# Performance work log

Measured on AMD Instinct MI355X. Metric: run time of the kernel, lower is better.

The kernel has to match this reference:

```python
import jax, jax.numpy as jnp
import numpy as np

N, E, G = 4096, 16384, 128   # nodes, edges, graphs
IN, H, ED = 64, 64, 16       # in_dim, hidden, edge_dim


def _lin(key, fan_in, fan_out):
    return jax.random.normal(key, (fan_in, fan_out), dtype=jnp.float32) * (fan_in ** -0.5)


def setup_inputs() -> dict:
    key = jax.random.key(0)
    ks = jax.random.split(key, 32)
    inp = {
        "x": jax.random.normal(ks[0], (N, IN), dtype=jnp.float32),
        "edge_index": jax.random.randint(ks[1], (2, E), 0, N, dtype=jnp.int32),
        "edge_attr": jax.random.normal(ks[2], (E, ED), dtype=jnp.float32),
        "batch": jnp.sort(jax.random.randint(ks[3], (N,), 0, G, dtype=jnp.int32)),
    }
    ki = 4
    dims = [(IN, H), (H, H), (H, H)]  # (in_channels, out_channels) per layer
    for l, (ic, oc) in enumerate(dims):
        hd = ic * oc  # edge-MLP width = hidden * in_channels
        inp[f"l{l}_w1"] = _lin(ks[ki], ED, hd); ki += 1
        inp[f"l{l}_b1"] = jnp.zeros((hd,), dtype=jnp.float32)
        inp[f"l{l}_w2"] = _lin(ks[ki], hd, hd); ki += 1
        inp[f"l{l}_b2"] = jnp.zeros((hd,), dtype=jnp.float32)
        inp[f"l{l}_root"] = _lin(ks[ki], ic, oc); ki += 1
        inp[f"l{l}_bias"] = jnp.zeros((oc,), dtype=jnp.float32)
    return inp


def _nnconv(x, src, dst, edge_attr, w1, b1, w2, b2, root, bias, ic, oc):
    # per-edge weight matrix Theta(e): [E, ic, oc]
    h = jax.nn.relu(edge_attr @ w1 + b1)
    theta = (h @ w2 + b2).reshape(-1, ic, oc)
    # gather source features, per-edge bmm, scatter-mean to target
    msg = jnp.einsum("ei,eio->eo", x[src], theta)
    agg = jax.ops.segment_sum(msg, dst, num_segments=N)
    cnt = jax.ops.segment_sum(jnp.ones((msg.shape[0],), msg.dtype), dst, num_segments=N)
    agg = agg / jnp.maximum(cnt, 1.0)[:, None]
    return agg + x @ root + bias


def reference(x, edge_index, edge_attr, batch,
              l0_w1, l0_b1, l0_w2, l0_b2, l0_root, l0_bias,
              l1_w1, l1_b1, l1_w2, l1_b2, l1_root, l1_bias,
              l2_w1, l2_b1, l2_w2, l2_b2, l2_root, l2_bias):
    src, dst = edge_index[0], edge_index[1]
    layers = [
        (l0_w1, l0_b1, l0_w2, l0_b2, l0_root, l0_bias, IN, H),
        (l1_w1, l1_b1, l1_w2, l1_b2, l1_root, l1_bias, H, H),
        (l2_w1, l2_b1, l2_w2, l2_b2, l2_root, l2_bias, H, H),
    ]
    h = x
    for (w1, b1, w2, b2, root, bias, ic, oc) in layers:
        h = jax.nn.relu(_nnconv(h, src, dst, edge_attr, w1, b1, w2, b2, root, bias, ic, oc))
        # dropout is identity in eval mode
    # global mean pool over graphs
    s = jax.ops.segment_sum(h, batch, num_segments=G)
    c = jax.ops.segment_sum(jnp.ones((N,), h.dtype), batch, num_segments=G)
    return s / jnp.maximum(c, 1.0)[:, None]
```

## Files before the change

kernel.cpp:

```cpp
#include <hip/hip_runtime.h>
#include <hip/hip_bf16.h>

#define NN 4096
#define EE 16384
#define GG 128
#define EDIM 16
#define HD 4096

#define NGROUPS 64
#define GK 8
#define KSUBS 64
#define MAXT 40
#define MAXSLOT (MAXT * 16)
#define MAXTW 5
#define SYHALF (64 * 64 * 8)

typedef __attribute__((ext_vector_type(8))) short short8;
typedef __attribute__((ext_vector_type(4))) float float4v;

static __device__ inline unsigned short f2b(float f) {
    unsigned u = __float_as_uint(f);
    unsigned r = u + 0x7fff + ((u >> 16) & 1);
    return (unsigned short)(r >> 16);
}

static __device__ inline unsigned pk2(float a, float b) {
    __hip_bfloat162 p = __float22bfloat162_rn(make_float2(a, b));
    return *(unsigned*)&p;
}

__global__ void hker(const float* __restrict__ ea, const float* __restrict__ w1,
                     const float* __restrict__ b1, unsigned short* __restrict__ hB) {
    __shared__ float sea[16 * 16];
    const int tid = threadIdx.x;
    const int j = blockIdx.x * 256 + tid;
    const int e0 = blockIdx.y * 16;
    float w[16];
#pragma unroll
    for (int k = 0; k < 16; ++k) w[k] = w1[k * HD + j];
    const float b = b1[j];
    sea[tid] = ea[e0 * EDIM + tid];
    __syncthreads();
#pragma unroll 4
    for (int el = 0; el < 16; ++el) {
        float a = b;
#pragma unroll
        for (int k = 0; k < 16; ++k) a += sea[el * 16 + k] * w[k];
        hB[(size_t)(e0 + el) * HD + j] = f2b(fmaxf(a, 0.f));
    }
}

__global__ void wperm(const float* __restrict__ w2, unsigned short* __restrict__ W2q) {
    __shared__ float t[64 * 65];
    const int k = blockIdx.x;
    const int tid = threadIdx.x;
    const int o = tid & 63, r4 = tid >> 6;
#pragma unroll
    for (int it = 0; it < 16; ++it) {
        int i = it * 4 + r4;
        t[i * 65 + o] = w2[(size_t)k * HD + i * 64 + o];
    }
    __syncthreads();
    const int o2 = tid >> 2, q = tid & 3;
    const int ss = k >> 3, kk = k & 7;
    size_t base = ((size_t)(ss * 512 + kk * 64 + o2)) * 64 + q * 16;
    unsigned int buf[8];
#pragma unroll
    for (int j = 0; j < 8; ++j)
        buf[j] = pk2(t[(q * 16 + 2 * j) * 65 + o2], t[(q * 16 + 2 * j + 1) * 65 + o2]);
    *(uint4*)(&W2q[base]) = make_uint4(buf[0], buf[1], buf[2], buf[3]);
    *(uint4*)(&W2q[base + 8]) = make_uint4(buf[4], buf[5], buf[6], buf[7]);
}

__global__ void count_edges(const int* __restrict__ src, const int* __restrict__ dst,
                            int* __restrict__ cnt_src, float* __restrict__ cnt_dst) {
    const int e = blockIdx.x * 256 + threadIdx.x;
    atomicAdd(&cnt_src[src[e]], 1);
    atomicAdd(&cnt_dst[dst[e]], 1.f);
}

__global__ void build_layout(const int* __restrict__ cnt_src, int* __restrict__ node_slot_base,
                             int* __restrict__ tile_cluster, int* __restrict__ group_ntiles) {
    const int g = threadIdx.x;
    int nt = 0;
    int slot = g * MAXSLOT;
    for (int c = 0; c < 16; ++c) {
        int d = 0;
        for (int j = 0; j < 4; ++j) {
            int n = g * 64 + c * 4 + j;
            node_slot_base[n] = slot + d;
            d += cnt_src[n];
        }
        int tcnt = (d + 15) >> 4;
        if (nt + tcnt > MAXT) tcnt = MAXT - nt;
        for (int j = 0; j < tcnt; ++j) tile_cluster[g * MAXT + nt + j] = c;
        nt += tcnt;
        slot += tcnt * 16;
    }
    group_ntiles[g] = nt;
}

__global__ void fill_slots(const int* __restrict__ src, const int* __restrict__ dst,
                           int* __restrict__ fill, const int* __restrict__ node_slot_base,
                           int* __restrict__ slot_info) {
    const int e = blockIdx.x * 256 + threadIdx.x;
    const int n = src[e];
    const int pos = atomicAdd(&fill[n], 1);
    const int s = node_slot_base[n] + pos;
    const int g = n >> 6;
    if (s < g * MAXSLOT + MAXSLOT)
        slot_info[s] = e | ((n & 3) << 14) | (dst[e] << 16);
}

__global__ void xb_ker(const float* __restrict__ xcur, const float* __restrict__ b2,
                       float* __restrict__ xb) {
    const int n = blockIdx.x * 4 + (threadIdx.x >> 6);
    const int o = threadIdx.x & 63;
    float a = 0.f;
#pragma unroll
    for (int i = 0; i < 64; ++i) a += xcur[n * 64 + i] * b2[i * 64 + o];
    xb[n * 64 + o] = a;
}

__global__ void b2scatter(const float* __restrict__ xb, const int* __restrict__ src,
                          const int* __restrict__ dst, float* __restrict__ agg) {
    const int e = blockIdx.x * 4 + (threadIdx.x >> 6);
    const int o = threadIdx.x & 63;
    atomicAdd(&agg[(size_t)dst[e] * 64 + o], xb[(size_t)src[e] * 64 + o]);
}

__global__ __launch_bounds__(512, 1)
void ygemm_msg(const float* __restrict__ xcur, const unsigned short* __restrict__ hB,
               const unsigned short* __restrict__ W2q, const int* __restrict__ slot_info,
               const int* __restrict__ tile_cluster, const int* __restrict__ group_ntiles,
               float* __restrict__ agg) {
    __shared__ __align__(16) unsigned short sA[64 * 72];
    __shared__ __align__(16) unsigned short sY[2 * SYHALF];

    const int bid = blockIdx.x;
    const int g = bid >> 3;
    const int kc = bid & 7;
    const int tid = threadIdx.x;
    const int lane = tid & 63, wave = tid >> 6;
    const int quad = lane >> 4, lm = lane & 15;

    {
        const int n = tid >> 3, ib = (tid & 7) * 8;
        const float* xp = xcur + (size_t)(g * 64 + n) * 64 + ib;
        uint4 w = make_uint4(pk2(xp[0], xp[1]), pk2(xp[2], xp[3]),
                             pk2(xp[4], xp[5]), pk2(xp[6], xp[7]));
        *(uint4*)(&sA[n * 72 + ib]) = w;
    }

    const int ntiles = group_ntiles[g];
    int infoR[MAXTW], tcR[MAXTW];
#pragma unroll
    for (int ai = 0; ai < MAXTW; ++ai) {
        const int ti = wave + ai * 8;
        infoR[ai] = (ti < ntiles) ? slot_info[g * MAXSLOT + ti * 16 + lm] : -1;
        tcR[ai]   = (ti < ntiles) ? tile_cluster[g * MAXT + ti] : 0;
    }

    float4v acc2[MAXTW][4];
#pragma unroll
    for (int a = 0; a < MAXTW; ++a)
#pragma unroll
        for (int t = 0; t < 4; ++t) {
            acc2[a][t][0] = 0.f; acc2[a][t][1] = 0.f;
            acc2[a][t][2] = 0.f; acc2[a][t][3] = 0.f;
        }

    const int qg = wave >> 1, half = wave & 1;
    __syncthreads();

    short8 af[4][2];
#pragma unroll
    for (int s = 0; s < 4; ++s)
#pragma unroll
        for (int q2 = 0; q2 < 2; ++q2)
            af[s][q2] = *(const short8*)(&sA[(s * 16 + lm) * 72 + q2 * 32 + quad * 8]);

    short8 bf[4][2];
    unsigned hd[MAXTW];
    {
        const size_t pan = (size_t)(kc * KSUBS) * 512;
#pragma unroll
        for (int tt = 0; tt < 4; ++tt)
#pragma unroll
            for (int q2 = 0; q2 < 2; ++q2)
                bf[tt][q2] = *(const short8*)(&W2q[(pan + wave * 64 + tt * 16 + lm) * 64 + q2 * 32 + quad * 8]);
        const int k0 = kc * KSUBS * 8;
#pragma unroll
        for (int ai = 0; ai < MAXTW; ++ai) {
            hd[ai] = 0;
            if (wave + ai * 8 < ntiles && infoR[ai] >= 0)
                hd[ai] = *(const unsigned*)(&hB[(size_t)(infoR[ai] & 0x3FFF) * HD + k0 + quad * 2]);
        }
    }

    for (int su = 0; su < KSUBS; ++su) {
        const int ss = kc * KSUBS + su;
        unsigned short* sYp = sY + (su & 1) * SYHALF;

#pragma unroll
        for (int s = 0; s < 4; ++s) {
            float4v a1[4];
#pragma unroll
            for (int tt = 0; tt < 4; ++tt) {
                a1[tt][0] = 0.f; a1[tt][1] = 0.f; a1[tt][2] = 0.f; a1[tt][3] = 0.f;
            }
#pragma unroll
            for (int q2 = 0; q2 < 2; ++q2)
#pragma unroll
                for (int tt = 0; tt < 4; ++tt)
                    a1[tt] = __builtin_amdgcn_mfma_f32_16x16x32_bf16(af[s][q2], bf[tt][q2], a1[tt], 0, 0, 0);
#pragma unroll
            for (int tt = 0; tt < 4; ++tt) {
                const int o = tt * 16 + lm;
                const int clqg = s * 16 + quad * 4 + qg;
                const int base = (o * 64 + (clqg ^ o)) * 8 + half * 4;
                uint2 v;
                v.x = pk2(a1[tt][0], a1[tt][1]);
                v.y = pk2(a1[tt][2], a1[tt][3]);
                *(uint2*)(&sYp[base]) = v;
            }
        }
        __syncthreads();

        const int sun = (su + 1 < KSUBS) ? su + 1 : su;
        const int ssn = kc * KSUBS + sun;
        short8 bfN[4][2];
        unsigned hdN[MAXTW];
        {
            const size_t pan = (size_t)ssn * 512;
#pragma unroll
            for (int tt = 0; tt < 4; ++tt)
#pragma unroll
                for (int q2 = 0; q2 < 2; ++q2)
                    bfN[tt][q2] = *(const short8*)(&W2q[(pan + wave * 64 + tt * 16 + lm) * 64 + q2 * 32 + quad * 8]);
            const int k0n = ssn * 8;
#pragma unroll
            for (int ai = 0; ai < MAXTW; ++ai) {
                hdN[ai] = 0;
                if (wave + ai * 8 < ntiles && infoR[ai] >= 0)
                    hdN[ai] = *(const unsigned*)(&hB[(size_t)(infoR[ai] & 0x3FFF) * HD + k0n + quad * 2]);
            }
        }

#pragma unroll
        for (int ai = 0; ai < MAXTW; ++ai) {
            const int ti = wave + ai * 8;
            if (ti < ntiles) {
                const int info = infoR[ai];
                const int nl = (info >> 14) & 3;
                const unsigned lo = hd[ai] & 0xffffu, hi = hd[ai] >> 16;
                unsigned w0 = nl == 0 ? lo : (nl == 1 ? (lo << 16) : 0u);
                unsigned w1 = nl == 2 ? lo : (nl == 3 ? (lo << 16) : 0u);
                unsigned w2v = nl == 0 ? hi : (nl == 1 ? (hi << 16) : 0u);
                unsigned w3 = nl == 2 ? hi : (nl == 3 ? (hi << 16) : 0u);
                uint4 aw = make_uint4(w0, w1, w2v, w3);
                short8 a2 = *(short8*)&aw;
                const int c4 = tcR[ai] * 4 + quad;
#pragma unroll
                for (int ot = 0; ot < 4; ++ot) {
                    const int o = ot * 16 + lm;
                    short8 b2f = *(const short8*)(&sYp[(o * 64 + (c4 ^ o)) * 8]);
                    acc2[ai][ot] = __builtin_amdgcn_mfma_f32_16x16x32_bf16(a2, b2f, acc2[ai][ot], 0, 0, 0);
                }
            }
        }

#pragma unroll
        for (int tt = 0; tt < 4; ++tt)
#pragma unroll
            for (int q2 = 0; q2 < 2; ++q2)
                bf[tt][q2] = bfN[tt][q2];
#pragma unroll
        for (int ai = 0; ai < MAXTW; ++ai) hd[ai] = hdN[ai];
    }

#pragma unroll
    for (int ai = 0; ai < MAXTW; ++ai) {
        const int ti = wave + ai * 8;
        if (ti < ntiles) {
#pragma unroll
            for (int r = 0; r < 4; ++r) {
                const int inf2 = __shfl(infoR[ai], quad * 4 + r, 64);
                if (inf2 >= 0) {
                    const int d = inf2 >> 16;
#pragma unroll
                    for (int ot = 0; ot < 4; ++ot)
                        atomicAdd(&agg[(size_t)d * 64 + ot * 16 + lm], acc2[ai][ot][r]);
                }
            }
        }
    }
}

__global__ void combine(const float* __restrict__ agg, const float* __restrict__ cnt,
                        const float* __restrict__ xcur, const float* __restrict__ root,
                        const float* __restrict__ bias, float* __restrict__ xn) {
    const int n = blockIdx.x * 4 + (threadIdx.x >> 6);
    const int o = threadIdx.x & 63;
    float a = agg[n * 64 + o] / fmaxf(cnt[n], 1.f);
    float r = bias[o];
#pragma unroll
    for (int i = 0; i < 64; ++i) r += xcur[n * 64 + i] * root[i * 64 + o];
    xn[n * 64 + o] = fmaxf(a + r, 0.f);
}

__global__ void pool_accum(const float* __restrict__ x3, const int* __restrict__ batch,
                           float* __restrict__ pool, float* __restrict__ pcnt) {
    const int n = blockIdx.x * 4 + (threadIdx.x >> 6);
    const int o = threadIdx.x & 63;
    const int gi = batch[n];
    atomicAdd(&pool[gi * 64 + o], x3[n * 64 + o]);
    if (o == 0) atomicAdd(&pcnt[gi], 1.f);
}

__global__ void pool_norm(const float* __restrict__ pool, const float* __restrict__ pcnt,
                          float* __restrict__ out) {
    const int idx = blockIdx.x * 256 + threadIdx.x;
    out[idx] = pool[idx] / fmaxf(pcnt[idx >> 6], 1.f);
}

extern "C" void kernel_launch(void* const* d_in, const int* in_sizes, int n_in,
                              void* d_out, int out_size, void* d_ws, size_t ws_size,
                              hipStream_t stream) {
    const float* x   = (const float*)d_in[0];
    const int*   ei  = (const int*)d_in[1];
    const float* ea  = (const float*)d_in[2];
    const int*   bat = (const int*)d_in[3];
    const int* srcp = ei;
    const int* dstp = ei + EE;

    char* ws = (char*)d_ws;
    size_t off = 0;
    unsigned short* hB  = (unsigned short*)(ws + off); off += (size_t)EE * HD * 2;
    unsigned short* W2q = (unsigned short*)(ws + off); off += (size_t)HD * HD * 2;
    int* slot_info      = (int*)(ws + off); off += (size_t)NGROUPS * MAXSLOT * 4;
    int* tile_cluster   = (int*)(ws + off); off += (size_t)NGROUPS * MAXT * 4;
    int* group_ntiles   = (int*)(ws + off); off += 1024;
    int* node_slot_base = (int*)(ws + off); off += (size_t)NN * 4;
    int* cnt_src        = (int*)(ws + off); off += (size_t)NN * 4;
    int* fillc          = (int*)(ws + off); off += (size_t)NN * 4;
    float* cnt_dst      = (float*)(ws + off); off += (size_t)NN * 4;
    float* agg  = (float*)(ws + off); off += (size_t)NN * 64 * 4;
    float* xb   = (float*)(ws + off); off += (size_t)NN * 64 * 4;
    float* xb0  = (float*)(ws + off); off += (size_t)NN * 64 * 4;
    float* xb1  = (float*)(ws + off); off += (size_t)NN * 64 * 4;
    float* pool = (float*)(ws + off); off += (size_t)GG * 64 * 4;
    float* pcnt = (float*)(ws + off); off += (size_t)GG * 4;

    hipMemsetAsync(slot_info, 0xFF, (size_t)NGROUPS * MAXSLOT * 4, stream);
    hipMemsetAsync(cnt_src, 0, (size_t)NN * 4 * 3, stream);
    count_edges<<<EE / 256, 256, 0, stream>>>(srcp, dstp, cnt_src, cnt_dst);
    build_layout<<<1, 64, 0, stream>>>(cnt_src, node_slot_base, tile_cluster, group_ntiles);
    fill_slots<<<EE / 256, 256, 0, stream>>>(srcp, dstp, fillc, node_slot_base, slot_info);

    const float* xcur = x;
    float* xbufs[2] = {xb0, xb1};

    for (int l = 0; l < 3; ++l) {
        const float* w1   = (const float*)d_in[4 + 6 * l + 0];
        const float* b1   = (const float*)d_in[4 + 6 * l + 1];
        const float* w2   = (const float*)d_in[4 + 6 * l + 2];
        const float* b2   = (const float*)d_in[4 + 6 * l + 3];
        const float* root = (const float*)d_in[4 + 6 * l + 4];
        const float* bias = (const float*)d_in[4 + 6 * l + 5];

        wperm<<<HD, 256, 0, stream>>>(w2, W2q);
        hker<<<dim3(HD / 256, EE / 16), 256, 0, stream>>>(ea, w1, b1, hB);
        xb_ker<<<NN / 4, 256, 0, stream>>>(xcur, b2, xb);
        hipMemsetAsync(agg, 0, (size_t)NN * 64 * 4, stream);
        b2scatter<<<EE / 4, 256, 0, stream>>>(xb, srcp, dstp, agg);
        ygemm_msg<<<NGROUPS * GK, 512, 0, stream>>>(xcur, hB, W2q, slot_info,
                                                    tile_cluster, group_ntiles, agg);
        float* xn = xbufs[l & 1];
        combine<<<NN / 4, 256, 0, stream>>>(agg, cnt_dst, xcur, root, bias, xn);
        xcur = xn;
    }
    hipMemsetAsync(pool, 0, (size_t)GG * 64 * 4 + (size_t)GG * 4, stream);
    pool_accum<<<NN / 4, 256, 0, stream>>>(xcur, bat, pool, pcnt);
    pool_norm<<<GG * 64 / 256, 256, 0, stream>>>(pool, pcnt, (float*)d_out);
}
```

Before: 1.666 ms.

## Re-layout W2 panels and LDS tiles to simplify addressing in fused message GEMM

Changes the W2 permutation so each lane loads its B fragments from contiguous memory with a running pointer, and replaces the XOR-swizzled LDS layout for the intermediate Y tile with a padded 65-stride layout using precomputed base offsets. Replaces the select chain that places the edge feature with a 64-bit shift. Routes invalid slots to a zeroed dummy hB row so the inner loop needs no branch, and manually double-buffers the prefetch registers via a lambda unrolled twice. Also raises launch_bounds to 2 blocks per CU, which may force register spills given the large accumulator arrays.

Result: slower. 1.703 ms (+2.2%).

```diff
diff --git a/kernel.cpp b/kernel.cpp
--- a/kernel.cpp
+++ b/kernel.cpp
@@ -13,7 +13,8 @@
 #define MAXT 40
 #define MAXSLOT (MAXT * 16)
 #define MAXTW 5
-#define SYHALF (64 * 64 * 8)
+#define SYUNITS (64 * 65 * 8)
+#define PANEL (8 * 64 * 64)
 
 typedef __attribute__((ext_vector_type(8))) short short8;
 typedef __attribute__((ext_vector_type(4))) float float4v;
@@ -62,14 +63,21 @@
     }
     __syncthreads();
     const int o2 = tid >> 2, q = tid & 3;
-    const int ss = k >> 3, kk = k & 7;
-    size_t base = ((size_t)(ss * 512 + kk * 64 + o2)) * 64 + q * 16;
-    unsigned int buf[8];
-#pragma unroll
-    for (int j = 0; j < 8; ++j)
-        buf[j] = pk2(t[(q * 16 + 2 * j) * 65 + o2], t[(q * 16 + 2 * j + 1) * 65 + o2]);
-    *(uint4*)(&W2q[base]) = make_uint4(buf[0], buf[1], buf[2], buf[3]);
-    *(uint4*)(&W2q[base + 8]) = make_uint4(buf[4], buf[5], buf[6], buf[7]);
+    const int q2 = q >> 1;
+    const int j0 = (o2 >> 4) * 2 + q2;
+    const int lmm = o2 & 15;
+    const int blk = k;
+#pragma unroll
+    for (int cc = 0; cc < 2; ++cc) {
+        const int quad = (q & 1) * 2 + cc;
+        const int ib = q * 16 + cc * 8;
+        size_t base = ((size_t)(blk * 64 + quad * 16 + lmm)) * 64 + j0 * 8;
+        unsigned b0 = pk2(t[(ib + 0) * 65 + o2], t[(ib + 1) * 65 + o2]);
+        unsigned b1 = pk2(t[(ib + 2) * 65 + o2], t[(ib + 3) * 65 + o2]);
+        unsigned b2_ = pk2(t[(ib + 4) * 65 + o2], t[(ib + 5) * 65 + o2]);
+        unsigned b3 = pk2(t[(ib + 6) * 65 + o2], t[(ib + 7) * 65 + o2]);
+        *(uint4*)(&W2q[base]) = make_uint4(b0, b1, b2_, b3);
+    }
 }
 
 __global__ void count_edges(const int* __restrict__ src, const int* __restrict__ dst,
@@ -129,13 +137,13 @@
     atomicAdd(&agg[(size_t)dst[e] * 64 + o], xb[(size_t)src[e] * 64 + o]);
 }
 
-__global__ __launch_bounds__(512, 1)
+__global__ __launch_bounds__(512, 2)
 void ygemm_msg(const float* __restrict__ xcur, const unsigned short* __restrict__ hB,
                const unsigned short* __restrict__ W2q, const int* __restrict__ slot_info,
                const int* __restrict__ tile_cluster, const int* __restrict__ group_ntiles,
                float* __restrict__ agg) {
     __shared__ __align__(16) unsigned short sA[64 * 72];
-    __shared__ __align__(16) unsigned short sY[2 * SYHALF];
+    __shared__ __align__(16) unsigned short sY[2 * SYUNITS];
 
     const int bid = blockIdx.x;
     const int g = bid >> 3;
@@ -153,12 +161,17 @@
     }
 
     const int ntiles = group_ntiles[g];
-    int infoR[MAXTW], tcR[MAXTW];
+    int infoR[MAXTW], voff[MAXTW], rbase[MAXTW];
+    unsigned shl5[MAXTW];
 #pragma unroll
     for (int ai = 0; ai < MAXTW; ++ai) {
         const int ti = wave + ai * 8;
-        infoR[ai] = (ti < ntiles) ? slot_info[g * MAXSLOT + ti * 16 + lm] : -1;
-        tcR[ai]   = (ti < ntiles) ? tile_cluster[g * MAXT + ti] : 0;
+        const int info = (ti < ntiles) ? slot_info[g * MAXSLOT + ti * 16 + lm] : -1;
+        const int tc   = (ti < ntiles) ? tile_cluster[g * MAXT + ti] : 0;
+        infoR[ai] = info;
+        voff[ai]  = ((info >= 0) ? (info & 0x3FFF) : EE) * HD + quad * 2;
+        rbase[ai] = ((tc * 4 + quad) * 65 + lm) * 8;
+        shl5[ai]  = (unsigned)(((info >> 14) & 3) * 16);
     }
 
     float4v acc2[MAXTW][4];
@@ -171,6 +184,7 @@
         }
 
     const int qg = wave >> 1, half = wave & 1;
+    const int wbase = ((quad * 4 + qg) * 65 + lm) * 8 + half * 4;
     __syncthreads();
 
     short8 af[4][2];
@@ -180,103 +194,77 @@
         for (int q2 = 0; q2 < 2; ++q2)
             af[s][q2] = *(const short8*)(&sA[(s * 16 + lm) * 72 + q2 * 32 + quad * 8]);
 
-    short8 bf[4][2];
-    unsigned hd[MAXTW];
-    {
-        const size_t pan = (size_t)(kc * KSUBS) * 512;
-#pragma unroll
-        for (int tt = 0; tt < 4; ++tt)
-#pragma unroll
-            for (int q2 = 0; q2 < 2; ++q2)
-                bf[tt][q2] = *(const short8*)(&W2q[(pan + wave * 64 + tt * 16 + lm) * 64 + q2 * 32 + quad * 8]);
-        const int k0 = kc * KSUBS * 8;
-#pragma unroll
-        for (int ai = 0; ai < MAXTW; ++ai) {
-            hd[ai] = 0;
-            if (wave + ai * 8 < ntiles && infoR[ai] >= 0)
-                hd[ai] = *(const unsigned*)(&hB[(size_t)(infoR[ai] & 0x3FFF) * HD + k0 + quad * 2]);
-        }
-    }
-
-    for (int su = 0; su < KSUBS; ++su) {
-        const int ss = kc * KSUBS + su;
-        unsigned short* sYp = sY + (su & 1) * SYHALF;
-
+    const float4v z4 = {0.f, 0.f, 0.f, 0.f};
+
+    const unsigned short* wp  = W2q + ((size_t)(kc * KSUBS * 8 + wave) * 64 + lane) * 64;
+    const unsigned short* hbk = hB + kc * KSUBS * 8;
+
+    short8 bfA[4][2], bfB[4][2];
+    unsigned hdA[MAXTW], hdB[MAXTW];
+#pragma unroll
+    for (int tt = 0; tt < 4; ++tt) {
+        bfA[tt][0] = *(const short8*)(wp + (tt * 2 + 0) * 8);
+        bfA[tt][1] = *(const short8*)(wp + (tt * 2 + 1) * 8);
+    }
+    wp += PANEL;
+#pragma unroll
+    for (int ai = 0; ai < MAXTW; ++ai) hdA[ai] = *(const unsigned*)(hbk + voff[ai]);
+    hbk += 8;
+
+    auto subody = [&](short8 (&BF)[4][2], unsigned (&HDc)[MAXTW],
+                      short8 (&BFN)[4][2], unsigned (&HDN)[MAXTW],
+                      unsigned short* __restrict__ sYp) {
 #pragma unroll
         for (int s = 0; s < 4; ++s) {
             float4v a1[4];
 #pragma unroll
+            for (int tt = 0; tt < 4; ++tt)
+                a1[tt] = __builtin_amdgcn_mfma_f32_16x16x32_bf16(af[s][0], BF[tt][0], z4, 0, 0, 0);
+#pragma unroll
+            for (int tt = 0; tt < 4; ++tt)
+                a1[tt] = __builtin_amdgcn_mfma_f32_16x16x32_bf16(af[s][1], BF[tt][1], a1[tt], 0, 0, 0);
+#pragma unroll
             for (int tt = 0; tt < 4; ++tt) {
-                a1[tt][0] = 0.f; a1[tt][1] = 0.f; a1[tt][2] = 0.f; a1[tt][3] = 0.f;
-            }
-#pragma unroll
-            for (int q2 = 0; q2 < 2; ++q2)
-#pragma unroll
-                for (int tt = 0; tt < 4; ++tt)
-                    a1[tt] = __builtin_amdgcn_mfma_f32_16x16x32_bf16(af[s][q2], bf[tt][q2], a1[tt], 0, 0, 0);
-#pragma unroll
-            for (int tt = 0; tt < 4; ++tt) {
-                const int o = tt * 16 + lm;
-                const int clqg = s * 16 + quad * 4 + qg;
-                const int base = (o * 64 + (clqg ^ o)) * 8 + half * 4;
                 uint2 v;
                 v.x = pk2(a1[tt][0], a1[tt][1]);
                 v.y = pk2(a1[tt][2], a1[tt][3]);
-                *(uint2*)(&sYp[base]) = v;
+                *(uint2*)(&sYp[wbase + s * 8320 + tt * 128]) = v;
             }
         }
         __syncthreads();
 
-        const int sun = (su + 1 < KSUBS) ? su + 1 : su;
-        const int ssn = kc * KSUBS + sun;
-        short8 bfN[4][2];
-        unsigned hdN[MAXTW];
-        {
-            const size_t pan = (size_t)ssn * 512;
-#pragma unroll
-            for (int tt = 0; tt < 4; ++tt)
-#pragma unroll
-                for (int q2 = 0; q2 < 2; ++q2)
-                    bfN[tt][q2] = *(const short8*)(&W2q[(pan + wave * 64 + tt * 16 + lm) * 64 + q2 * 32 + quad * 8]);
-            const int k0n = ssn * 8;
-#pragma unroll
-            for (int ai = 0; ai < MAXTW; ++ai) {
-                hdN[ai] = 0;
-                if (wave + ai * 8 < ntiles && infoR[ai] >= 0)
-                    hdN[ai] = *(const unsigned*)(&hB[(size_t)(infoR[ai] & 0x3FFF) * HD + k0n + quad * 2]);
-            }
-        }
+#pragma unroll
+        for (int tt = 0; tt < 4; ++tt) {
+            BFN[tt][0] = *(const short8*)(wp + (tt * 2 + 0) * 8);
+            BFN[tt][1] = *(const short8*)(wp + (tt * 2 + 1) * 8);
+        }
+        wp += PANEL;
+#pragma unroll
+        for (int ai = 0; ai < MAXTW; ++ai)
+            HDN[ai] = *(const unsigned*)(hbk + voff[ai]);
+        hbk += 8;
 
 #pragma unroll
         for (int ai = 0; ai < MAXTW; ++ai) {
-            const int ti = wave + ai * 8;
-            if (ti < ntiles) {
-                const int info = infoR[ai];
-                const int nl = (info >> 14) & 3;
-                const unsigned lo = hd[ai] & 0xffffu, hi = hd[ai] >> 16;
-                unsigned w0 = nl == 0 ? lo : (nl == 1 ? (lo << 16) : 0u);
-                unsigned w1 = nl == 2 ? lo : (nl == 3 ? (lo << 16) : 0u);
-                unsigned w2v = nl == 0 ? hi : (nl == 1 ? (hi << 16) : 0u);
-                unsigned w3 = nl == 2 ? hi : (nl == 3 ? (hi << 16) : 0u);
-                uint4 aw = make_uint4(w0, w1, w2v, w3);
+            if (wave + ai * 8 < ntiles) {
+                const unsigned h0 = HDc[ai];
+                unsigned long long A = (unsigned long long)(h0 & 0xffffu) << shl5[ai];
+                unsigned long long B = (unsigned long long)(h0 >> 16) << shl5[ai];
+                uint4 aw = make_uint4((unsigned)A, (unsigned)(A >> 32),
+                                      (unsigned)B, (unsigned)(B >> 32));
                 short8 a2 = *(short8*)&aw;
-                const int c4 = tcR[ai] * 4 + quad;
 #pragma unroll
                 for (int ot = 0; ot < 4; ++ot) {
-                    const int o = ot * 16 + lm;
-                    short8 b2f = *(const short8*)(&sYp[(o * 64 + (c4 ^ o)) * 8]);
+                    short8 b2f = *(const short8*)(&sYp[rbase[ai] + ot * 128]);
                     acc2[ai][ot] = __builtin_amdgcn_mfma_f32_16x16x32_bf16(a2, b2f, acc2[ai][ot], 0, 0, 0);
                 }
             }
         }
-
-#pragma unroll
-        for (int tt = 0; tt < 4; ++tt)
-#pragma unroll
-            for (int q2 = 0; q2 < 2; ++q2)
-                bf[tt][q2] = bfN[tt][q2];
-#pragma unroll
-        for (int ai = 0; ai < MAXTW; ++ai) hd[ai] = hdN[ai];
+    };
+
+    for (int su2 = 0; su2 < KSUBS; su2 += 2) {
+        subody(bfA, hdA, bfB, hdB, sY);
+        subody(bfB, hdB, bfA, hdA, sY + SYUNITS);
     }
 
 #pragma unroll
@@ -336,8 +324,8 @@
 
     char* ws = (char*)d_ws;
     size_t off = 0;
-    unsigned short* hB  = (unsigned short*)(ws + off); off += (size_t)EE * HD * 2;
-    unsigned short* W2q = (unsigned short*)(ws + off); off += (size_t)HD * HD * 2;
+    unsigned short* hB  = (unsigned short*)(ws + off); off += (size_t)(EE + 1) * HD * 2;
+    unsigned short* W2q = (unsigned short*)(ws + off); off += ((size_t)HD * HD + PANEL) * 2;
     int* slot_info      = (int*)(ws + off); off += (size_t)NGROUPS * MAXSLOT * 4;
     int* tile_cluster   = (int*)(ws + off); off += (size_t)NGROUPS * MAXT * 4;
     int* group_ntiles   = (int*)(ws + off); off += 1024;
@@ -354,6 +342,7 @@
 
     hipMemsetAsync(slot_info, 0xFF, (size_t)NGROUPS * MAXSLOT * 4, stream);
     hipMemsetAsync(cnt_src, 0, (size_t)NN * 4 * 3, stream);
+    hipMemsetAsync(hB + (size_t)EE * HD, 0, (size_t)HD * 2, stream);
     count_edges<<<EE / 256, 256, 0, stream>>>(srcp, dstp, cnt_src, cnt_dst);
     build_layout<<<1, 64, 0, stream>>>(cnt_src, node_slot_base, tile_cluster, group_ntiles);
     fill_slots<<<EE / 256, 256, 0, stream>>>(srcp, dstp, fillc, node_slot_base, slot_info);
```
